# Kernel optimization log

Hardware: AMD Instinct MI355X
Metric: run time of the kernel (lower is better)

Reference implementation:

```python
import jax, jax.numpy as jnp
import numpy as np

N, E, D_IN, H, OUT = 50000, 800000, 128, 256, 2
BN_EPS = 1e-5
LN_EPS = 1e-5


def _xavier(k, fi, fo):
    lim = float(np.sqrt(6.0 / (fi + fo)))
    return jax.random.uniform(k, (fi, fo), minval=-lim, maxval=lim, dtype=jnp.float32)


def setup_inputs() -> dict:
    key = jax.random.key(0)
    ks = jax.random.split(key, 8)
    return {
        "x": jax.random.normal(ks[0], (N, D_IN), dtype=jnp.float32),
        "edge_index": jax.random.randint(ks[1], (2, E), 0, N, dtype=jnp.int32),
        "feature_scale": jnp.ones((D_IN,), jnp.float32),
        "feature_bias": jnp.zeros((D_IN,), jnp.float32),
        "bn0_g": jnp.ones((D_IN,), jnp.float32),
        "bn0_b": jnp.zeros((D_IN,), jnp.float32),
        "W1": _xavier(ks[2], D_IN, H), "b1": jnp.zeros((H,), jnp.float32),
        "bn1_g": jnp.ones((H,), jnp.float32), "bn1_b": jnp.zeros((H,), jnp.float32),
        "ln1_g": jnp.ones((H,), jnp.float32), "ln1_b": jnp.zeros((H,), jnp.float32),
        "W2": _xavier(ks[3], H, H), "b2": jnp.zeros((H,), jnp.float32),
        "bn2_g": jnp.ones((H,), jnp.float32), "bn2_b": jnp.zeros((H,), jnp.float32),
        "ln2_g": jnp.ones((H,), jnp.float32), "ln2_b": jnp.zeros((H,), jnp.float32),
        "Wout": _xavier(ks[4], H, OUT), "bout": jnp.zeros((OUT,), jnp.float32),
    }


def _batchnorm(x, g, b):
    # training-mode BatchNorm1d: batch stats over node axis, biased variance
    mu = jnp.mean(x, axis=0)
    var = jnp.mean(jnp.square(x - mu), axis=0)
    return g * (x - mu) * jax.lax.rsqrt(var + BN_EPS) + b


def _layernorm(x, g, b):
    mu = jnp.mean(x, axis=-1, keepdims=True)
    var = jnp.mean(jnp.square(x - mu), axis=-1, keepdims=True)
    return g * (x - mu) * jax.lax.rsqrt(var + LN_EPS) + b


def _gcn(x, W, b, src, dst, dinv):
    # PyG GCNConv with self-loops: D^{-1/2}(A+I)D^{-1/2} X W + b
    h = x @ W                                   # [N, F]
    norm = (dinv[src] * dinv[dst])[:, None]     # [E, 1]
    msg = h[src] * norm                         # [E, F] (dominant traffic)
    agg = jax.ops.segment_sum(msg, dst, num_segments=N)
    return agg + (dinv * dinv)[:, None] * h + b


def _forward(x, feature_scale, feature_bias, bn0_g, bn0_b,
             W1, b1, bn1_g, bn1_b, ln1_g, ln1_b,
             W2, b2, bn2_g, bn2_b, ln2_g, ln2_b,
             Wout, bout, edge_index):
    src, dst = edge_index[0], edge_index[1]
    deg = jax.ops.segment_sum(jnp.ones((E,), x.dtype), dst, num_segments=N) + 1.0
    dinv = jax.lax.rsqrt(deg)

    h = x * feature_scale + feature_bias
    h = _batchnorm(h, bn0_g, bn0_b)            # input_bn; dropout = identity (eval)

    # layer 0 (no residual: i == 0)
    h1 = _gcn(h, W1, b1, src, dst, dinv)
    h1 = jax.nn.relu(h1)
    h1 = _batchnorm(h1, bn1_g, bn1_b)
    h1 = _layernorm(h1, ln1_g, ln1_b)

    # layer 1 (residual add, shapes match)
    h2 = _gcn(h1, W2, b2, src, dst, dinv)
    h2 = jax.nn.relu(h2)
    h2 = _batchnorm(h2, bn2_g, bn2_b)
    h2 = _layernorm(h2, ln2_g, ln2_b)
    h2 = h2 + h1

    return h2 @ Wout + bout


def reference(x, edge_index, feature_scale, feature_bias, bn0_g, bn0_b,
              W1, b1, bn1_g, bn1_b, ln1_g, ln1_b,
              W2, b2, bn2_g, bn2_b, ln2_g, ln2_b,
              Wout, bout):
    return _forward(x, feature_scale, feature_bias, bn0_g, bn0_b,
                    W1, b1, bn1_g, bn1_b, ln1_g, ln1_b,
                    W2, b2, bn2_g, bn2_b, ln2_g, ln2_b,
                    Wout, bout, edge_index)
```

## Files before the change

kernel.cpp:

```cpp
#include <hip/hip_runtime.h>
#include <hip/hip_bf16.h>
#include <stdint.h>

#define N_NODES 50000
#define N_EDGES 800000
#define D_IN    128
#define H_DIM   256
#define BN_EPS  1e-5f
#define LN_EPS  1e-5f
#define NBLK2 782
#define SLICE_ELEMS ((size_t)N_NODES * 32)
#define EDGE_CHUNK 4096
#define BN0_BLOCKS 1024
#define PREPX_BLOCKS 6250
#define TR_BLOCKS 256
#define NBKT 196
#define CHUNK 2048
#define RCHUNKS 391

typedef float v4f __attribute__((ext_vector_type(4)));
typedef float v2f __attribute__((ext_vector_type(2)));
typedef short v8s __attribute__((ext_vector_type(8)));
typedef unsigned v4u __attribute__((ext_vector_type(4)));

__device__ __forceinline__ float bflo(unsigned u){ return __uint_as_float(u << 16); }
__device__ __forceinline__ float bfhi(unsigned u){ return __uint_as_float(u & 0xffff0000u); }
__device__ __forceinline__ unsigned short f2bf(float f){
  unsigned u = __float_as_uint(f);
  u += 0x7fffu + ((u >> 16) & 1u);
  return (unsigned short)(u >> 16);
}
__device__ __forceinline__ unsigned pack2(float a, float b){
  return (unsigned)f2bf(a) | ((unsigned)f2bf(b) << 16);
}

__device__ __forceinline__ int block_excl_scan(int v){
  int t = threadIdx.x;
  int lane = t & 63, w = t >> 6;
  int inc = v;
  #pragma unroll
  for (int m = 1; m < 64; m <<= 1){
    int o = __shfl_up(inc, m, 64);
    if (lane >= m) inc += o;
  }
  __shared__ int wsum[4];
  if (lane == 63) wsum[w] = inc;
  __syncthreads();
  int base = 0;
  #pragma unroll
  for (int j = 0; j < 4; ++j) if (j < w) base += wsum[j];
  return base + inc - v;
}

__global__ __launch_bounds__(256) void bn0r1_k(const int* ei, const float* x,
                                               const float* fs, const float* fb,
                                               float* S, float* Q, int* ghist){
  int b = blockIdx.x, t = threadIdx.x;
  if (b >= BN0_BLOCKS){
    __shared__ int lh[NBKT];
    int b2 = b - BN0_BLOCKS;
    for (int i = t; i < NBKT; i += 256) lh[i] = 0;
    __syncthreads();
    int e0 = b2 * CHUNK;
    int n = min(CHUNK, N_EDGES - e0);
    for (int i = t; i < n; i += 256)
      atomicAdd(&lh[ei[N_EDGES + e0 + i] >> 8], 1);
    __syncthreads();
    if (t < NBKT && lh[t] > 0) atomicAdd(&ghist[t], lh[t]);
    return;
  }
  int cl = t & 31, rg = t >> 5;
  int c = cl * 4;
  float4 fs4 = *(const float4*)(fs + c);
  float4 fb4 = *(const float4*)(fb + c);
  float s0=0,s1=0,s2=0,s3=0,q0=0,q1=0,q2=0,q3=0;
  for (int row = b * 8 + rg; row < N_NODES; row += BN0_BLOCKS * 8){
    float4 xv = *(const float4*)(x + (size_t)row * D_IN + c);
    float v0 = xv.x * fs4.x + fb4.x;
    float v1 = xv.y * fs4.y + fb4.y;
    float v2 = xv.z * fs4.z + fb4.z;
    float v3 = xv.w * fs4.w + fb4.w;
    s0 += v0; s1 += v1; s2 += v2; s3 += v3;
    q0 += v0*v0; q1 += v1*v1; q2 += v2*v2; q3 += v3*v3;
  }
  __shared__ float red[256][8];
  red[t][0]=s0; red[t][1]=s1; red[t][2]=s2; red[t][3]=s3;
  red[t][4]=q0; red[t][5]=q1; red[t][6]=q2; red[t][7]=q3;
  __syncthreads();
  float* Sr = S + (b & 7) * D_IN;
  float* Qr = Q + (b & 7) * D_IN;
  if (t < 32){
    float a[8];
    #pragma unroll
    for (int i = 0; i < 8; ++i) a[i] = red[t][i];
    for (int j = 1; j < 8; ++j)
      #pragma unroll
      for (int i = 0; i < 8; ++i) a[i] += red[t + 32*j][i];
    #pragma unroll
    for (int i = 0; i < 4; ++i){ atomicAdd(&Sr[t*4+i], a[i]); atomicAdd(&Qr[t*4+i], a[4+i]); }
  }
}

__global__ __launch_bounds__(256) void r3_k(const int* ei, const int* ghist, int* gcursor, unsigned* ebuf){
  __shared__ unsigned short dstS[CHUNK];
  __shared__ int lh[NBKT], cb[NBKT], sbb[NBKT];
  int t = threadIdx.x;
  int v = (t < NBKT) ? ghist[t] : 0;
  int epre = block_excl_scan(v);
  if (t < NBKT){ sbb[t] = epre; lh[t] = 0; }
  __syncthreads();
  int e0 = blockIdx.x * CHUNK;
  int n = min(CHUNK, N_EDGES - e0);
  for (int i = t; i < n; i += 256){
    int d = ei[N_EDGES + e0 + i];
    dstS[i] = (unsigned short)d;
    atomicAdd(&lh[d >> 8], 1);
  }
  __syncthreads();
  if (t < NBKT && lh[t] > 0) cb[t] = sbb[t] + atomicAdd(&gcursor[t], lh[t]);
  __syncthreads();
  if (t < NBKT) lh[t] = 0;
  __syncthreads();
  for (int i = t; i < n; i += 256){
    int d = dstS[i];
    int bkt = d >> 8;
    int r = atomicAdd(&lh[bkt], 1);
    unsigned src = (unsigned)ei[e0 + i];
    ebuf[cb[bkt] + r] = ((unsigned)(d & 255) << 16) | src;
  }
}

__global__ __launch_bounds__(256) void sortprep_k(const unsigned* ebuf, const int* ghist,
                                                  int* perm, int* offs, float* dinv,
                                                  unsigned short* edges,
                                                  const float* x, const float* S, const float* Q,
                                                  const float* fs, const float* fb,
                                                  const float* gg, const float* bb,
                                                  unsigned short* xt,
                                                  const float* W1, const float* W2,
                                                  unsigned short* W1t, unsigned short* W2t){
  int b = blockIdx.x, t = threadIdx.x;
  if (b < NBKT){
    __shared__ int h[256], dh[128], ep_s[128], W_s[128], lc[128], curs[256], sbb[NBKT + 1];
    int gv = (t < NBKT) ? ghist[t] : 0;
    int gpre = block_excl_scan(gv);
    if (t < NBKT) sbb[t] = gpre;
    if (t == NBKT - 1) sbb[NBKT] = gpre + gv;
    h[t] = 0;
    if (t < 128){ dh[t] = 0; lc[t] = 0; }
    __syncthreads();
    int lo = sbb[b], hi = sbb[b + 1];
    for (int i = lo + t; i < hi; i += 256)
      atomicAdd(&h[(ebuf[i] >> 16) & 255], 1);
    __syncthreads();
    int node = b * 256 + t;
    bool valid = node < N_NODES;
    int deg = valid ? h[t] : 0;
    if (valid) atomicAdd(&dh[min(deg, 127)], 1);
    __syncthreads();
    int cv = (t < 128) ? dh[t] : 0;
    int e1 = block_excl_scan(cv);
    __syncthreads();
    int e2 = block_excl_scan((t < 128) ? cv * t : 0);
    __syncthreads();
    if (t < 128){ ep_s[t] = e1; W_s[t] = e2; }
    __syncthreads();
    if (valid){
      int bin = min(deg, 127);
      int r = atomicAdd(&lc[bin], 1);
      int pl = ep_s[bin] + r;
      int pos = b * 256 + pl;
      int off = lo + W_s[bin] + (pl - ep_s[bin]) * deg;
      perm[pos] = node;
      offs[pos] = off;
      dinv[node] = rsqrtf((float)deg + 1.0f);
      curs[t] = off;
    }
    __syncthreads();
    for (int i = lo + t; i < hi; i += 256){
      unsigned u = ebuf[i];
      int l8 = (u >> 16) & 255;
      int pos = atomicAdd(&curs[l8], 1);
      edges[pos] = (unsigned short)(u & 0xffffu);
    }
    if (b == 0 && t == 0) offs[N_NODES] = N_EDGES;
    return;
  }
  if (b < NBKT + PREPX_BLOCKS){
    int i = (b - NBKT) * 256 + t;
    int row = i >> 5; int c = (i & 31) * 4;
    float4 Sv = *(const float4*)(S + c);
    float4 Qv = *(const float4*)(Q + c);
    #pragma unroll
    for (int rep = 1; rep < 8; ++rep){
      float4 s2 = *(const float4*)(S + rep * D_IN + c);
      float4 q2 = *(const float4*)(Q + rep * D_IN + c);
      Sv.x += s2.x; Sv.y += s2.y; Sv.z += s2.z; Sv.w += s2.w;
      Qv.x += q2.x; Qv.y += q2.y; Qv.z += q2.z; Qv.w += q2.w;
    }
    float4 fs4 = *(const float4*)(fs + c);
    float4 fb4 = *(const float4*)(fb + c);
    float4 gg4 = *(const float4*)(gg + c);
    float4 bb4 = *(const float4*)(bb + c);
    const float invN = 1.0f / N_NODES;
    float mu0 = Sv.x*invN, mu1 = Sv.y*invN, mu2 = Sv.z*invN, mu3 = Sv.w*invN;
    float r0 = rsqrtf(Qv.x*invN - mu0*mu0 + BN_EPS);
    float r1 = rsqrtf(Qv.y*invN - mu1*mu1 + BN_EPS);
    float r2 = rsqrtf(Qv.z*invN - mu2*mu2 + BN_EPS);
    float r3 = rsqrtf(Qv.w*invN - mu3*mu3 + BN_EPS);
    float a0 = gg4.x*r0*fs4.x, c0 = gg4.x*r0*(fb4.x - mu0) + bb4.x;
    float a1 = gg4.y*r1*fs4.y, c1 = gg4.y*r1*(fb4.y - mu1) + bb4.y;
    float a2 = gg4.z*r2*fs4.z, c2 = gg4.z*r2*(fb4.z - mu2) + bb4.z;
    float a3 = gg4.w*r3*fs4.w, c3 = gg4.w*r3*(fb4.w - mu3) + bb4.w;
    float4 xv = *(const float4*)(x + (size_t)row * D_IN + c);
    uint2 o;
    o.x = pack2(a0 * xv.x + c0, a1 * xv.y + c1);
    o.y = pack2(a2 * xv.z + c2, a3 * xv.w + c3);
    *(uint2*)(xt + (size_t)row * D_IN + c) = o;
    return;
  }
  int i = (b - NBKT - PREPX_BLOCKS) * 256 + t;
  if (i < D_IN * H_DIM){
    int r = i / H_DIM, c = i % H_DIM;
    W1t[c * D_IN + r] = f2bf(W1[i]);
  }
  if (i < H_DIM * H_DIM){
    int r = i / H_DIM, c = i % H_DIM;
    W2t[c * H_DIM + r] = f2bf(W2[i]);
  }
}

template<int K>
__global__ __launch_bounds__(256) void gemm_k(const unsigned short* A, const unsigned short* Bt,
                                              const float* dinv, unsigned short* C, int M){
  __shared__ __align__(16) short smem[16896];
  __shared__ float dvs[64];
  short* As = smem;
  short* Bs = smem + 64 * 40;
  int t = threadIdx.x;
  int m0 = blockIdx.x * 64;
  int lane = t & 63;
  int w = t >> 6;
  int fr = lane & 15, quad = lane >> 4;
  if (t < 64) dvs[t] = (m0 + t < M) ? dinv[m0 + t] : 0.0f;
  v4f acc[4][4] = {};
  int sr = t >> 2;
  int sk = (t & 3) << 3;
  for (int k0 = 0; k0 < K; k0 += 32){
    __syncthreads();
    uint4 av = {0,0,0,0};
    int arow = m0 + sr;
    if (arow < M) av = *(const uint4*)(A + (size_t)arow * K + k0 + sk);
    *(uint4*)(&As[sr * 40 + sk]) = av;
    #pragma unroll
    for (int j = 0; j < 4; ++j){
      int brow = sr + 64 * j;
      uint4 bv = *(const uint4*)(Bt + (size_t)brow * K + k0 + sk);
      *(uint4*)(&Bs[brow * 40 + sk]) = bv;
    }
    __syncthreads();
    v8s af[4], bf[4];
    #pragma unroll
    for (int mi = 0; mi < 4; ++mi)
      af[mi] = *(const v8s*)(&As[(mi * 16 + fr) * 40 + quad * 8]);
    #pragma unroll
    for (int ni = 0; ni < 4; ++ni)
      bf[ni] = *(const v8s*)(&Bs[(w * 64 + ni * 16 + fr) * 40 + quad * 8]);
    #pragma unroll
    for (int mi = 0; mi < 4; ++mi)
      #pragma unroll
      for (int ni = 0; ni < 4; ++ni)
        acc[mi][ni] = __builtin_amdgcn_mfma_f32_16x16x32_bf16(af[mi], bf[ni], acc[mi][ni], 0, 0, 0);
  }
  __syncthreads();
  short* Cs = smem;
  #pragma unroll
  for (int mi = 0; mi < 4; ++mi)
    #pragma unroll
    for (int ni = 0; ni < 4; ++ni)
      #pragma unroll
      for (int r = 0; r < 4; ++r){
        int row = mi * 16 + quad * 4 + r;
        int col = w * 64 + ni * 16 + fr;
        Cs[row * 264 + col] = (short)f2bf(acc[mi][ni][r] * dvs[row]);
      }
  __syncthreads();
  int orow = t >> 2;
  int grow = m0 + orow;
  if (grow < M){
    #pragma unroll
    for (int j = 0; j < 4; ++j){
      int oc = (t & 3) * 16 + 64 * j;
      v8s v0 = *(const v8s*)(&Cs[orow * 264 + oc]);
      v8s v1 = *(const v8s*)(&Cs[orow * 264 + oc + 8]);
      *(v8s*)(&C[(size_t)(oc >> 5) * SLICE_ELEMS + (size_t)grow * 32 + (oc & 31)]) = v0;
      int oc1 = oc + 8;
      *(v8s*)(&C[(size_t)(oc1 >> 5) * SLICE_ELEMS + (size_t)grow * 32 + (oc1 & 31)]) = v1;
    }
  }
}

#define ACCP(u, A) { v2f d_ = {bflo(u), bfhi(u)}; A += d_; }
#define ACC8(vv) ACCP(vv.x, A0) ACCP(vv.y, A1) ACCP(vv.z, A2) ACCP(vv.w, A3)

__global__ __launch_bounds__(256, 4) void agg_k(const unsigned short* hs, const int* offsets,
                                                const unsigned short* edges, const int* perm,
                                                const float* dinv, const float* bias,
                                                unsigned short* g, float* pS, float* pQ){
  __shared__ unsigned eds32[EDGE_CHUNK / 2];
  __shared__ float wps[4][4][16];
  int t = threadIdx.x;
  int lane = t & 63;
  int wv = t >> 6;
  int slice = blockIdx.x & 7;
  int l4 = lane & 3;
  int grp = blockIdx.x >> 3;
  int nb = grp * 64;
  int idx = nb + (t >> 2);
  int lastn = min(nb + 64, N_NODES);
  int blk0 = offsets[nb];
  int base = blk0 & ~1;
  int blkN = offsets[lastn];
  const unsigned* gsrc = (const unsigned*)(edges + base);
  int nu = min((blkN - base + 1) >> 1, EDGE_CHUNK / 2);
  for (int i = t; i < nu; i += 256)
    eds32[i] = gsrc[i];
  __syncthreads();
  bool act = idx < N_NODES;
  int node = act ? perm[idx] : 0;
  float dvv = act ? dinv[node] : 0.f;
  const uint4* hb4 = (const uint4*)(hs + (size_t)slice * SLICE_ELEMS);
  float4 bb0 = *(const float4*)(bias + slice * 32 + l4 * 8);
  float4 bb1 = *(const float4*)(bias + slice * 32 + l4 * 8 + 4);
  uint4 sv = hb4[(size_t)node * 4 + l4];
  v2f A0 = {bflo(sv.x), bfhi(sv.x)};
  v2f A1 = {bflo(sv.y), bfhi(sv.y)};
  v2f A2 = {bflo(sv.z), bfhi(sv.z)};
  v2f A3 = {bflo(sv.w), bfhi(sv.w)};
  int e  = act ? offsets[idx] : 0;
  int e1 = act ? offsets[idx + 1] : 0;
  if ((e & 1) && e < e1){
    int ru = (e - base) >> 1;
    unsigned d = (ru < EDGE_CHUNK / 2) ? eds32[ru] : gsrc[ru];
    uint4 vv = hb4[(size_t)(d >> 16) * 4 + l4];
    ACC8(vv);
    ++e;
  }
  for (; e + 16 <= e1; e += 16){
    int ru = (e - base) >> 1;
    unsigned dd[8];
    if (ru + 8 <= EDGE_CHUNK / 2){
      #pragma unroll
      for (int j = 0; j < 8; ++j) dd[j] = eds32[ru + j];
    } else {
      #pragma unroll
      for (int j = 0; j < 8; ++j) dd[j] = gsrc[ru + j];
    }
    uint4 v[16];
    #pragma unroll
    for (int j = 0; j < 8; ++j){
      v[2*j]   = hb4[(size_t)(dd[j] & 0xffffu) * 4 + l4];
      v[2*j+1] = hb4[(size_t)(dd[j] >> 16)     * 4 + l4];
    }
    #pragma unroll
    for (int j = 0; j < 16; ++j){ ACC8(v[j]); }
  }
  if (e + 8 <= e1){
    int ru = (e - base) >> 1;
    unsigned dd[4];
    if (ru + 4 <= EDGE_CHUNK / 2){
      #pragma unroll
      for (int j = 0; j < 4; ++j) dd[j] = eds32[ru + j];
    } else {
      #pragma unroll
      for (int j = 0; j < 4; ++j) dd[j] = gsrc[ru + j];
    }
    uint4 v[8];
    #pragma unroll
    for (int j = 0; j < 4; ++j){
      v[2*j]   = hb4[(size_t)(dd[j] & 0xffffu) * 4 + l4];
      v[2*j+1] = hb4[(size_t)(dd[j] >> 16)     * 4 + l4];
    }
    #pragma unroll
    for (int j = 0; j < 8; ++j){ ACC8(v[j]); }
    e += 8;
  }
  if (e + 4 <= e1){
    int ru = (e - base) >> 1;
    unsigned dd0, dd1;
    if (ru + 2 <= EDGE_CHUNK / 2){
      dd0 = eds32[ru]; dd1 = eds32[ru + 1];
    } else {
      dd0 = gsrc[ru]; dd1 = gsrc[ru + 1];
    }
    uint4 v[4];
    v[0] = hb4[(size_t)(dd0 & 0xffffu) * 4 + l4];
    v[1] = hb4[(size_t)(dd0 >> 16)     * 4 + l4];
    v[2] = hb4[(size_t)(dd1 & 0xffffu) * 4 + l4];
    v[3] = hb4[(size_t)(dd1 >> 16)     * 4 + l4];
    #pragma unroll
    for (int j = 0; j < 4; ++j){ ACC8(v[j]); }
    e += 4;
  }
  for (; e < e1; ++e){
    int r = e - base;
    unsigned d = ((r >> 1) < EDGE_CHUNK / 2) ? eds32[r >> 1] : gsrc[r >> 1];
    unsigned s = (r & 1) ? (d >> 16) : (d & 0xffffu);
    uint4 vv = hb4[(size_t)s * 4 + l4];
    ACC8(vv);
  }
  float y0 = act ? fmaxf(dvv * A0.x + bb0.x, 0.f) : 0.f;
  float y1 = act ? fmaxf(dvv * A0.y + bb0.y, 0.f) : 0.f;
  float y2 = act ? fmaxf(dvv * A1.x + bb0.z, 0.f) : 0.f;
  float y3 = act ? fmaxf(dvv * A1.y + bb0.w, 0.f) : 0.f;
  float y4 = act ? fmaxf(dvv * A2.x + bb1.x, 0.f) : 0.f;
  float y5 = act ? fmaxf(dvv * A2.y + bb1.y, 0.f) : 0.f;
  float y6 = act ? fmaxf(dvv * A3.x + bb1.z, 0.f) : 0.f;
  float y7 = act ? fmaxf(dvv * A3.y + bb1.w, 0.f) : 0.f;
  if (act){
    v4u o;
    o.x = pack2(y0, y1); o.y = pack2(y2, y3);
    o.z = pack2(y4, y5); o.w = pack2(y6, y7);
    __builtin_nontemporal_store(o, (v4u*)(g + (size_t)node * H_DIM + slice * 32 + l4 * 8));
  }
  float q0 = y0*y0, q1 = y1*y1, q2 = y2*y2, q3 = y3*y3;
  float q4 = y4*y4, q5 = y5*y5, q6 = y6*y6, q7 = y7*y7;
  #pragma unroll
  for (int m = 4; m < 64; m <<= 1){
    y0 += __shfl_xor(y0, m, 64); y1 += __shfl_xor(y1, m, 64);
    y2 += __shfl_xor(y2, m, 64); y3 += __shfl_xor(y3, m, 64);
    y4 += __shfl_xor(y4, m, 64); y5 += __shfl_xor(y5, m, 64);
    y6 += __shfl_xor(y6, m, 64); y7 += __shfl_xor(y7, m, 64);
    q0 += __shfl_xor(q0, m, 64); q1 += __shfl_xor(q1, m, 64);
    q2 += __shfl_xor(q2, m, 64); q3 += __shfl_xor(q3, m, 64);
    q4 += __shfl_xor(q4, m, 64); q5 += __shfl_xor(q5, m, 64);
    q6 += __shfl_xor(q6, m, 64); q7 += __shfl_xor(q7, m, 64);
  }
  if (lane < 4){
    wps[wv][lane][0] = y0; wps[wv][lane][1] = y1; wps[wv][lane][2] = y2; wps[wv][lane][3] = y3;
    wps[wv][lane][4] = y4; wps[wv][lane][5] = y5; wps[wv][lane][6] = y6; wps[wv][lane][7] = y7;
    wps[wv][lane][8] = q0; wps[wv][lane][9] = q1; wps[wv][lane][10] = q2; wps[wv][lane][11] = q3;
    wps[wv][lane][12] = q4; wps[wv][lane][13] = q5; wps[wv][lane][14] = q6; wps[wv][lane][15] = q7;
  }
  __syncthreads();
  if (t < 64){
    int tl = t >> 4, ti = t & 15;
    float v = wps[0][tl][ti] + wps[1][tl][ti] + wps[2][tl][ti] + wps[3][tl][ti];
    int col32 = tl * 8 + (ti & 7);
    if (ti < 8) pS[(size_t)blockIdx.x * 32 + col32] = v;
    else        pQ[(size_t)blockIdx.x * 32 + col32] = v;
  }
}

__global__ __launch_bounds__(1024) void redu_k(const float* pS, const float* pQ,
                                               float* Sg, float* Qg){
  __shared__ float ls[32][32], lq[32][32];
  int t = threadIdx.x;
  int slice = blockIdx.x & 7;
  int part = blockIdx.x >> 3;
  int grp = t >> 5, c32 = t & 31;
  float as = 0.f, aq = 0.f;
  for (int b2 = part + grp * 8; b2 < NBLK2; b2 += 256){
    size_t o = ((size_t)b2 * 8 + slice) * 32 + c32;
    as += pS[o]; aq += pQ[o];
  }
  ls[grp][c32] = as; lq[grp][c32] = aq;
  __syncthreads();
  if (t < 32){
    float S = 0.f, Q = 0.f;
    #pragma unroll
    for (int gI = 0; gI < 32; ++gI){ S += ls[gI][t]; Q += lq[gI][t]; }
    atomicAdd(&Sg[slice * 32 + t], S);
    atomicAdd(&Qg[slice * 32 + t], Q);
  }
}

__global__ __launch_bounds__(256) void apply1_k(const unsigned short* g,
                                                const float* Sg, const float* Qg,
                                                const float* bng, const float* bnb,
                                                const float* lng, const float* lnb, unsigned short* h1){
  int t = threadIdx.x;
  int lane32 = t & 31;
  int row = blockIdx.x * 8 + (t >> 5);
  if (row >= N_NODES) return;
  int c = lane32 * 8;
  const float invN = 1.0f / N_NODES;
  float4 S0 = *(const float4*)(Sg + c), S1 = *(const float4*)(Sg + c + 4);
  float4 Q0 = *(const float4*)(Qg + c), Q1 = *(const float4*)(Qg + c + 4);
  float4 G0 = *(const float4*)(bng + c), G1 = *(const float4*)(bng + c + 4);
  float4 B0 = *(const float4*)(bnb + c), B1 = *(const float4*)(bnb + c + 4);
  float Sa[8] = {S0.x,S0.y,S0.z,S0.w,S1.x,S1.y,S1.z,S1.w};
  float Qa[8] = {Q0.x,Q0.y,Q0.z,Q0.w,Q1.x,Q1.y,Q1.z,Q1.w};
  float Ga[8] = {G0.x,G0.y,G0.z,G0.w,G1.x,G1.y,G1.z,G1.w};
  float Ba[8] = {B0.x,B0.y,B0.z,B0.w,B1.x,B1.y,B1.z,B1.w};
  float scv[8], shv[8];
  #pragma unroll
  for (int j = 0; j < 8; ++j){
    float mu = Sa[j] * invN;
    float rs = rsqrtf(Qa[j] * invN - mu * mu + BN_EPS);
    float s = Ga[j] * rs;
    scv[j] = s; shv[j] = Ba[j] - s * mu;
  }
  uint4 u = *(const uint4*)(g + (size_t)row * H_DIM + c);
  float v0 = scv[0] * bflo(u.x) + shv[0];
  float v1 = scv[1] * bfhi(u.x) + shv[1];
  float v2 = scv[2] * bflo(u.y) + shv[2];
  float v3 = scv[3] * bfhi(u.y) + shv[3];
  float v4 = scv[4] * bflo(u.z) + shv[4];
  float v5 = scv[5] * bfhi(u.z) + shv[5];
  float v6 = scv[6] * bflo(u.w) + shv[6];
  float v7 = scv[7] * bfhi(u.w) + shv[7];
  float sum = v0+v1+v2+v3+v4+v5+v6+v7;
  float sq  = v0*v0+v1*v1+v2*v2+v3*v3+v4*v4+v5*v5+v6*v6+v7*v7;
  #pragma unroll
  for (int m = 1; m < 32; m <<= 1){ sum += __shfl_xor(sum, m, 64); sq += __shfl_xor(sq, m, 64); }
  float mu = sum * (1.0f / H_DIM);
  float var = sq * (1.0f / H_DIM) - mu * mu;
  float rs = rsqrtf(var + LN_EPS);
  float4 g40 = *(const float4*)(lng + c);
  float4 g41 = *(const float4*)(lng + c + 4);
  float4 b40 = *(const float4*)(lnb + c);
  float4 b41 = *(const float4*)(lnb + c + 4);
  uint4 o;
  o.x = pack2(g40.x * (v0 - mu) * rs + b40.x, g40.y * (v1 - mu) * rs + b40.y);
  o.y = pack2(g40.z * (v2 - mu) * rs + b40.z, g40.w * (v3 - mu) * rs + b40.w);
  o.z = pack2(g41.x * (v4 - mu) * rs + b41.x, g41.y * (v5 - mu) * rs + b41.y);
  o.w = pack2(g41.z * (v6 - mu) * rs + b41.z, g41.w * (v7 - mu) * rs + b41.w);
  *(uint4*)(h1 + (size_t)row * H_DIM + c) = o;
}

__global__ __launch_bounds__(256) void apply2_k(const unsigned short* g,
                                                const float* Sg, const float* Qg,
                                                const float* bng, const float* bnb,
                                                const float* lng, const float* lnb,
                                                const unsigned short* h1, const float* Wout,
                                                const float* bout, float* out){
  int t = threadIdx.x;
  int lane32 = t & 31;
  int row = blockIdx.x * 8 + (t >> 5);
  if (row >= N_NODES) return;
  int c = lane32 * 8;
  const float invN = 1.0f / N_NODES;
  float4 S0 = *(const float4*)(Sg + c), S1 = *(const float4*)(Sg + c + 4);
  float4 Q0 = *(const float4*)(Qg + c), Q1 = *(const float4*)(Qg + c + 4);
  float4 G0 = *(const float4*)(bng + c), G1 = *(const float4*)(bng + c + 4);
  float4 B0 = *(const float4*)(bnb + c), B1 = *(const float4*)(bnb + c + 4);
  float Sa[8] = {S0.x,S0.y,S0.z,S0.w,S1.x,S1.y,S1.z,S1.w};
  float Qa[8] = {Q0.x,Q0.y,Q0.z,Q0.w,Q1.x,Q1.y,Q1.z,Q1.w};
  float Ga[8] = {G0.x,G0.y,G0.z,G0.w,G1.x,G1.y,G1.z,G1.w};
  float Ba[8] = {B0.x,B0.y,B0.z,B0.w,B1.x,B1.y,B1.z,B1.w};
  float scv[8], shv[8];
  #pragma unroll
  for (int j = 0; j < 8; ++j){
    float mu = Sa[j] * invN;
    float rs = rsqrtf(Qa[j] * invN - mu * mu + BN_EPS);
    float s = Ga[j] * rs;
    scv[j] = s; shv[j] = Ba[j] - s * mu;
  }
  uint4 u = *(const uint4*)(g + (size_t)row * H_DIM + c);
  float v0 = scv[0] * bflo(u.x) + shv[0];
  float v1 = scv[1] * bfhi(u.x) + shv[1];
  float v2 = scv[2] * bflo(u.y) + shv[2];
  float v3 = scv[3] * bfhi(u.y) + shv[3];
  float v4 = scv[4] * bflo(u.z) + shv[4];
  float v5 = scv[5] * bfhi(u.z) + shv[5];
  float v6 = scv[6] * bflo(u.w) + shv[6];
  float v7 = scv[7] * bfhi(u.w) + shv[7];
  float sum = v0+v1+v2+v3+v4+v5+v6+v7;
  float sq  = v0*v0+v1*v1+v2*v2+v3*v3+v4*v4+v5*v5+v6*v6+v7*v7;
  #pragma unroll
  for (int m = 1; m < 32; m <<= 1){ sum += __shfl_xor(sum, m, 64); sq += __shfl_xor(sq, m, 64); }
  float mu = sum * (1.0f / H_DIM);
  float var = sq * (1.0f / H_DIM) - mu * mu;
  float rs = rsqrtf(var + LN_EPS);
  float4 g40 = *(const float4*)(lng + c);
  float4 g41 = *(const float4*)(lng + c + 4);
  float4 b40 = *(const float4*)(lnb + c);
  float4 b41 = *(const float4*)(lnb + c + 4);
  uint4 hr = *(const uint4*)(h1 + (size_t)row * H_DIM + c);
  float y0 = g40.x * (v0 - mu) * rs + b40.x + bflo(hr.x);
  float y1 = g40.y * (v1 - mu) * rs + b40.y + bfhi(hr.x);
  float y2 = g40.z * (v2 - mu) * rs + b40.z + bflo(hr.y);
  float y3 = g40.w * (v3 - mu) * rs + b40.w + bfhi(hr.y);
  float y4 = g41.x * (v4 - mu) * rs + b41.x + bflo(hr.z);
  float y5 = g41.y * (v5 - mu) * rs + b41.y + bfhi(hr.z);
  float y6 = g41.z * (v6 - mu) * rs + b41.z + bflo(hr.w);
  float y7 = g41.w * (v7 - mu) * rs + b41.w + bfhi(hr.w);
  float4 w0 = *(const float4*)(Wout + c * 2);
  float4 w1 = *(const float4*)(Wout + c * 2 + 4);
  float4 w2 = *(const float4*)(Wout + c * 2 + 8);
  float4 w3 = *(const float4*)(Wout + c * 2 + 12);
  float o0 = y0*w0.x + y1*w0.z + y2*w1.x + y3*w1.z + y4*w2.x + y5*w2.z + y6*w3.x + y7*w3.z;
  float o1 = y0*w0.y + y1*w0.w + y2*w1.y + y3*w1.w + y4*w2.y + y5*w2.w + y6*w3.y + y7*w3.w;
  #pragma unroll
  for (int m = 1; m < 32; m <<= 1){ o0 += __shfl_xor(o0, m, 64); o1 += __shfl_xor(o1, m, 64); }
  if (lane32 == 0){
    out[(size_t)row * 2 + 0] = o0 + bout[0];
    out[(size_t)row * 2 + 1] = o1 + bout[1];
  }
}

extern "C" void kernel_launch(void* const* d_in, const int* in_sizes, int n_in,
                              void* d_out, int out_size, void* d_ws, size_t ws_size,
                              hipStream_t stream) {
  const float* x    = (const float*)d_in[0];
  const int*   ei   = (const int*)d_in[1];
  const float* fs   = (const float*)d_in[2];
  const float* fb   = (const float*)d_in[3];
  const float* bn0g = (const float*)d_in[4];
  const float* bn0b = (const float*)d_in[5];
  const float* W1   = (const float*)d_in[6];
  const float* b1   = (const float*)d_in[7];
  const float* bn1g = (const float*)d_in[8];
  const float* bn1b = (const float*)d_in[9];
  const float* ln1g = (const float*)d_in[10];
  const float* ln1b = (const float*)d_in[11];
  const float* W2   = (const float*)d_in[12];
  const float* b2   = (const float*)d_in[13];
  const float* bn2g = (const float*)d_in[14];
  const float* bn2b = (const float*)d_in[15];
  const float* ln2g = (const float*)d_in[16];
  const float* ln2b = (const float*)d_in[17];
  const float* Wout = (const float*)d_in[18];
  const float* bout = (const float*)d_in[19];
  float* out = (float*)d_out;

  char* w = (char*)d_ws;
  float* bn0S  = (float*)(w + 0);
  float* bn0Q  = (float*)(w + 4096);
  int*   ghist  = (int*)(w + 8192);
  int*   gcursor= (int*)(w + 8976);
  float* Sg1   = (float*)(w + 9760);
  float* Qg1   = (float*)(w + 10784);
  float* Sg2   = (float*)(w + 11808);
  float* Qg2   = (float*)(w + 12832);
  const size_t ZERO_BYTES = 13856;
  float* dinv  = (float*)(w + 211584);
  int*   offs  = (int*)(w + 411584);
  int*   perm  = (int*)(w + 611712);
  unsigned short* edges = (unsigned short*)(w + 1011712);
  unsigned short* xt   = (unsigned short*)(w + 2611712);
  unsigned short* W1t  = (unsigned short*)(w + 15411712);
  unsigned short* W2t  = (unsigned short*)(w + 15477248);
  unsigned short* hlin = (unsigned short*)(w + 15608320);
  unsigned*       ebuf = (unsigned*)(w + 15608320);
  unsigned short* gbuf = (unsigned short*)(w + 41208320);
  unsigned short* h1   = (unsigned short*)(w + 66808320);
  float* pS    = (float*)(w + 92408320);
  float* pQ    = (float*)(w + 94008832);

  (void)in_sizes; (void)n_in; (void)out_size; (void)ws_size;

  hipMemsetAsync(d_ws, 0, ZERO_BYTES, stream);

  bn0r1_k<<<BN0_BLOCKS + RCHUNKS, 256, 0, stream>>>(ei, x, fs, fb, bn0S, bn0Q, ghist);
  r3_k<<<RCHUNKS, 256, 0, stream>>>(ei, ghist, gcursor, ebuf);
  sortprep_k<<<NBKT + PREPX_BLOCKS + TR_BLOCKS, 256, 0, stream>>>(
      ebuf, ghist, perm, offs, dinv, edges, x, bn0S, bn0Q, fs, fb, bn0g, bn0b, xt, W1, W2, W1t, W2t);

  int ggrid = (N_NODES + 63) / 64;
  int agg_blocks = NBLK2 * 8;

  gemm_k<D_IN><<<ggrid, 256, 0, stream>>>(xt, W1t, dinv, hlin, N_NODES);
  agg_k<<<agg_blocks, 256, 0, stream>>>(hlin, offs, edges, perm, dinv, b1, gbuf, pS, pQ);
  redu_k<<<64, 1024, 0, stream>>>(pS, pQ, Sg1, Qg1);
  apply1_k<<<(N_NODES + 7) / 8, 256, 0, stream>>>(gbuf, Sg1, Qg1, bn1g, bn1b, ln1g, ln1b, h1);

  gemm_k<H_DIM><<<ggrid, 256, 0, stream>>>(h1, W2t, dinv, hlin, N_NODES);
  agg_k<<<agg_blocks, 256, 0, stream>>>(hlin, offs, edges, perm, dinv, b2, gbuf, pS, pQ);
  redu_k<<<64, 1024, 0, stream>>>(pS, pQ, Sg2, Qg2);
  apply2_k<<<(N_NODES + 7) / 8, 256, 0, stream>>>(gbuf, Sg2, Qg2, bn2g, bn2b, ln2g, ln2b, h1, Wout, bout, out);
}
```

Before: 337.8 us.

## Fuse input BN prep into GEMM1 and BN/LN apply into GEMM2 prologue

The separate pass that normalised x into a bf16 buffer is removed, and GEMM1 now loads fp32 x, applies the folded scale and bias, and stages the whole 64x128 A tile in shared memory. The apply1 kernel is removed too. GEMM2 now reads the aggregated rows, applies BatchNorm and LayerNorm in its prologue, keeps the full 64x256 A tile in LDS, and also writes h1 for the later residual. This removes two kernel launches and the write and re-read of intermediate buffers, at the cost of larger LDS use per block (lower occupancy) and heavy per-thread register use in the GEMM2 prologue.

```diff
diff --git a/kernel.cpp b/kernel.cpp
--- a/kernel.cpp
+++ b/kernel.cpp
@@ -12,7 +12,6 @@
 #define SLICE_ELEMS ((size_t)N_NODES * 32)
 #define EDGE_CHUNK 4096
 #define BN0_BLOCKS 1024
-#define PREPX_BLOCKS 6250
 #define TR_BLOCKS 256
 #define NBKT 196
 #define CHUNK 2048
@@ -133,10 +132,6 @@
 __global__ __launch_bounds__(256) void sortprep_k(const unsigned* ebuf, const int* ghist,
                                                   int* perm, int* offs, float* dinv,
                                                   unsigned short* edges,
-                                                  const float* x, const float* S, const float* Q,
-                                                  const float* fs, const float* fb,
-                                                  const float* gg, const float* bb,
-                                                  unsigned short* xt,
                                                   const float* W1, const float* W2,
                                                   unsigned short* W1t, unsigned short* W2t){
   int b = blockIdx.x, t = threadIdx.x;
@@ -186,40 +181,7 @@
     if (b == 0 && t == 0) offs[N_NODES] = N_EDGES;
     return;
   }
-  if (b < NBKT + PREPX_BLOCKS){
-    int i = (b - NBKT) * 256 + t;
-    int row = i >> 5; int c = (i & 31) * 4;
-    float4 Sv = *(const float4*)(S + c);
-    float4 Qv = *(const float4*)(Q + c);
-    #pragma unroll
-    for (int rep = 1; rep < 8; ++rep){
-      float4 s2 = *(const float4*)(S + rep * D_IN + c);
-      float4 q2 = *(const float4*)(Q + rep * D_IN + c);
-      Sv.x += s2.x; Sv.y += s2.y; Sv.z += s2.z; Sv.w += s2.w;
-      Qv.x += q2.x; Qv.y += q2.y; Qv.z += q2.z; Qv.w += q2.w;
-    }
-    float4 fs4 = *(const float4*)(fs + c);
-    float4 fb4 = *(const float4*)(fb + c);
-    float4 gg4 = *(const float4*)(gg + c);
-    float4 bb4 = *(const float4*)(bb + c);
-    const float invN = 1.0f / N_NODES;
-    float mu0 = Sv.x*invN, mu1 = Sv.y*invN, mu2 = Sv.z*invN, mu3 = Sv.w*invN;
-    float r0 = rsqrtf(Qv.x*invN - mu0*mu0 + BN_EPS);
-    float r1 = rsqrtf(Qv.y*invN - mu1*mu1 + BN_EPS);
-    float r2 = rsqrtf(Qv.z*invN - mu2*mu2 + BN_EPS);
-    float r3 = rsqrtf(Qv.w*invN - mu3*mu3 + BN_EPS);
-    float a0 = gg4.x*r0*fs4.x, c0 = gg4.x*r0*(fb4.x - mu0) + bb4.x;
-    float a1 = gg4.y*r1*fs4.y, c1 = gg4.y*r1*(fb4.y - mu1) + bb4.y;
-    float a2 = gg4.z*r2*fs4.z, c2 = gg4.z*r2*(fb4.z - mu2) + bb4.z;
-    float a3 = gg4.w*r3*fs4.w, c3 = gg4.w*r3*(fb4.w - mu3) + bb4.w;
-    float4 xv = *(const float4*)(x + (size_t)row * D_IN + c);
-    uint2 o;
-    o.x = pack2(a0 * xv.x + c0, a1 * xv.y + c1);
-    o.y = pack2(a2 * xv.z + c2, a3 * xv.w + c3);
-    *(uint2*)(xt + (size_t)row * D_IN + c) = o;
-    return;
-  }
-  int i = (b - NBKT - PREPX_BLOCKS) * 256 + t;
+  int i = (b - NBKT) * 256 + t;
   if (i < D_IN * H_DIM){
     int r = i / H_DIM, c = i % H_DIM;
     W1t[c * D_IN + r] = f2bf(W1[i]);
@@ -230,39 +192,194 @@
   }
 }
 
-template<int K>
-__global__ __launch_bounds__(256) void gemm_k(const unsigned short* A, const unsigned short* Bt,
-                                              const float* dinv, unsigned short* C, int M){
-  __shared__ __align__(16) short smem[16896];
-  __shared__ float dvs[64];
+__global__ __launch_bounds__(256) void gemm1_k(const float* x, const float* S, const float* Q,
+                                               const float* fs, const float* fb,
+                                               const float* gg, const float* bb,
+                                               const unsigned short* Bt, const float* dinv,
+                                               unsigned short* C, int M){
+  __shared__ __align__(16) short smem[18944];
+  __shared__ float ac[128], cc[128], dvs[64];
   short* As = smem;
-  short* Bs = smem + 64 * 40;
+  short* Bs = smem + 64 * 136;
   int t = threadIdx.x;
   int m0 = blockIdx.x * 64;
-  int lane = t & 63;
-  int w = t >> 6;
+  int lane = t & 63, w = t >> 6;
   int fr = lane & 15, quad = lane >> 4;
   if (t < 64) dvs[t] = (m0 + t < M) ? dinv[m0 + t] : 0.0f;
+  if (t < 128){
+    float s8 = 0.f, q8 = 0.f;
+    #pragma unroll
+    for (int rep = 0; rep < 8; ++rep){ s8 += S[rep * D_IN + t]; q8 += Q[rep * D_IN + t]; }
+    const float invN = 1.0f / N_NODES;
+    float mu = s8 * invN;
+    float rs = rsqrtf(q8 * invN - mu * mu + BN_EPS);
+    float a = gg[t] * rs * fs[t];
+    ac[t] = a;
+    cc[t] = gg[t] * rs * (fb[t] - mu) + bb[t];
+  }
+  __syncthreads();
+  {
+    int r = t >> 2, q = t & 3;
+    int arow = m0 + r;
+    #pragma unroll
+    for (int j = 0; j < 4; ++j){
+      int c = q * 32 + j * 8;
+      float4 xv0 = {0,0,0,0}, xv1 = {0,0,0,0};
+      if (arow < M){
+        xv0 = *(const float4*)(x + (size_t)arow * D_IN + c);
+        xv1 = *(const float4*)(x + (size_t)arow * D_IN + c + 4);
+      }
+      float4 a0 = *(const float4*)(&ac[c]);
+      float4 a1 = *(const float4*)(&ac[c + 4]);
+      float4 c0 = *(const float4*)(&cc[c]);
+      float4 c1 = *(const float4*)(&cc[c + 4]);
+      uint4 o;
+      o.x = pack2(a0.x * xv0.x + c0.x, a0.y * xv0.y + c0.y);
+      o.y = pack2(a0.z * xv0.z + c0.z, a0.w * xv0.w + c0.w);
+      o.z = pack2(a1.x * xv1.x + c1.x, a1.y * xv1.y + c1.y);
+      o.w = pack2(a1.z * xv1.z + c1.z, a1.w * xv1.w + c1.w);
+      *(uint4*)(&As[r * 136 + c]) = o;
+    }
+  }
   v4f acc[4][4] = {};
   int sr = t >> 2;
   int sk = (t & 3) << 3;
-  for (int k0 = 0; k0 < K; k0 += 32){
-    __syncthreads();
-    uint4 av = {0,0,0,0};
-    int arow = m0 + sr;
-    if (arow < M) av = *(const uint4*)(A + (size_t)arow * K + k0 + sk);
-    *(uint4*)(&As[sr * 40 + sk]) = av;
+  for (int k0 = 0; k0 < D_IN; k0 += 32){
+    __syncthreads();
     #pragma unroll
     for (int j = 0; j < 4; ++j){
       int brow = sr + 64 * j;
-      uint4 bv = *(const uint4*)(Bt + (size_t)brow * K + k0 + sk);
+      uint4 bv = *(const uint4*)(Bt + (size_t)brow * D_IN + k0 + sk);
       *(uint4*)(&Bs[brow * 40 + sk]) = bv;
     }
     __syncthreads();
     v8s af[4], bf[4];
     #pragma unroll
     for (int mi = 0; mi < 4; ++mi)
-      af[mi] = *(const v8s*)(&As[(mi * 16 + fr) * 40 + quad * 8]);
+      af[mi] = *(const v8s*)(&As[(mi * 16 + fr) * 136 + k0 + quad * 8]);
+    #pragma unroll
+    for (int ni = 0; ni < 4; ++ni)
+      bf[ni] = *(const v8s*)(&Bs[(w * 64 + ni * 16 + fr) * 40 + quad * 8]);
+    #pragma unroll
+    for (int mi = 0; mi < 4; ++mi)
+      #pragma unroll
+      for (int ni = 0; ni < 4; ++ni)
+        acc[mi][ni] = __builtin_amdgcn_mfma_f32_16x16x32_bf16(af[mi], bf[ni], acc[mi][ni], 0, 0, 0);
+  }
+  __syncthreads();
+  short* Cs = smem;
+  #pragma unroll
+  for (int mi = 0; mi < 4; ++mi)
+    #pragma unroll
+    for (int ni = 0; ni < 4; ++ni)
+      #pragma unroll
+      for (int r = 0; r < 4; ++r){
+        int row = mi * 16 + quad * 4 + r;
+        int col = w * 64 + ni * 16 + fr;
+        Cs[row * 264 + col] = (short)f2bf(acc[mi][ni][r] * dvs[row]);
+      }
+  __syncthreads();
+  int orow = t >> 2;
+  int grow = m0 + orow;
+  if (grow < M){
+    #pragma unroll
+    for (int j = 0; j < 4; ++j){
+      int oc = (t & 3) * 16 + 64 * j;
+      v8s v0 = *(const v8s*)(&Cs[orow * 264 + oc]);
+      v8s v1 = *(const v8s*)(&Cs[orow * 264 + oc + 8]);
+      *(v8s*)(&C[(size_t)(oc >> 5) * SLICE_ELEMS + (size_t)grow * 32 + (oc & 31)]) = v0;
+      int oc1 = oc + 8;
+      *(v8s*)(&C[(size_t)(oc1 >> 5) * SLICE_ELEMS + (size_t)grow * 32 + (oc1 & 31)]) = v1;
+    }
+  }
+}
+
+__global__ __launch_bounds__(256) void gemm2_k(const unsigned short* gB,
+                                               const float* Sg, const float* Qg,
+                                               const float* bng, const float* bnb,
+                                               const float* lng, const float* lnb,
+                                               const unsigned short* Bt, const float* dinv,
+                                               unsigned short* C, unsigned short* h1, int M){
+  __shared__ __align__(16) short smem[27136];
+  __shared__ float scs[256], shs[256], dvs[64];
+  short* As = smem;
+  short* Bs = smem + 64 * 264;
+  int t = threadIdx.x;
+  int m0 = blockIdx.x * 64;
+  int lane = t & 63, w = t >> 6;
+  int fr = lane & 15, quad = lane >> 4;
+  if (t < 64) dvs[t] = (m0 + t < M) ? dinv[m0 + t] : 0.0f;
+  {
+    const float invN = 1.0f / N_NODES;
+    float mu = Sg[t] * invN;
+    float rs = rsqrtf(Qg[t] * invN - mu * mu + BN_EPS);
+    float s = bng[t] * rs;
+    scs[t] = s; shs[t] = bnb[t] - s * mu;
+  }
+  __syncthreads();
+  {
+    int r = t >> 2, q = t & 3;
+    int grow = m0 + r;
+    int c0 = q * 64;
+    float v[64];
+    #pragma unroll
+    for (int j = 0; j < 8; ++j){
+      uint4 u = {0,0,0,0};
+      int c = c0 + j * 8;
+      if (grow < M) u = *(const uint4*)(gB + (size_t)grow * H_DIM + c);
+      float4 s0 = *(const float4*)(&scs[c]);
+      float4 s1 = *(const float4*)(&scs[c + 4]);
+      float4 h0 = *(const float4*)(&shs[c]);
+      float4 h4 = *(const float4*)(&shs[c + 4]);
+      v[j*8+0] = s0.x * bflo(u.x) + h0.x;
+      v[j*8+1] = s0.y * bfhi(u.x) + h0.y;
+      v[j*8+2] = s0.z * bflo(u.y) + h0.z;
+      v[j*8+3] = s0.w * bfhi(u.y) + h0.w;
+      v[j*8+4] = s1.x * bflo(u.z) + h4.x;
+      v[j*8+5] = s1.y * bfhi(u.z) + h4.y;
+      v[j*8+6] = s1.z * bflo(u.w) + h4.z;
+      v[j*8+7] = s1.w * bfhi(u.w) + h4.w;
+    }
+    float sum = 0.f, sq = 0.f;
+    #pragma unroll
+    for (int i = 0; i < 64; ++i){ sum += v[i]; sq += v[i] * v[i]; }
+    sum += __shfl_xor(sum, 1, 64); sum += __shfl_xor(sum, 2, 64);
+    sq  += __shfl_xor(sq, 1, 64);  sq  += __shfl_xor(sq, 2, 64);
+    float mu = sum * (1.0f / H_DIM);
+    float var = sq * (1.0f / H_DIM) - mu * mu;
+    float rs = rsqrtf(var + LN_EPS);
+    #pragma unroll
+    for (int j = 0; j < 8; ++j){
+      int c = c0 + j * 8;
+      float4 g0 = *(const float4*)(lng + c);
+      float4 g1 = *(const float4*)(lng + c + 4);
+      float4 b0 = *(const float4*)(lnb + c);
+      float4 b1 = *(const float4*)(lnb + c + 4);
+      uint4 o;
+      o.x = pack2(g0.x * (v[j*8+0] - mu) * rs + b0.x, g0.y * (v[j*8+1] - mu) * rs + b0.y);
+      o.y = pack2(g0.z * (v[j*8+2] - mu) * rs + b0.z, g0.w * (v[j*8+3] - mu) * rs + b0.w);
+      o.z = pack2(g1.x * (v[j*8+4] - mu) * rs + b1.x, g1.y * (v[j*8+5] - mu) * rs + b1.y);
+      o.w = pack2(g1.z * (v[j*8+6] - mu) * rs + b1.z, g1.w * (v[j*8+7] - mu) * rs + b1.w);
+      *(uint4*)(&As[r * 264 + c]) = o;
+      if (grow < M) *(uint4*)(h1 + (size_t)grow * H_DIM + c) = o;
+    }
+  }
+  v4f acc[4][4] = {};
+  int sr = t >> 2;
+  int sk = (t & 3) << 3;
+  for (int k0 = 0; k0 < H_DIM; k0 += 32){
+    __syncthreads();
+    #pragma unroll
+    for (int j = 0; j < 4; ++j){
+      int brow = sr + 64 * j;
+      uint4 bv = *(const uint4*)(Bt + (size_t)brow * H_DIM + k0 + sk);
+      *(uint4*)(&Bs[brow * 40 + sk]) = bv;
+    }
+    __syncthreads();
+    v8s af[4], bf[4];
+    #pragma unroll
+    for (int mi = 0; mi < 4; ++mi)
+      af[mi] = *(const v8s*)(&As[(mi * 16 + fr) * 264 + k0 + quad * 8]);
     #pragma unroll
     for (int ni = 0; ni < 4; ++ni)
       bf[ni] = *(const v8s*)(&Bs[(w * 64 + ni * 16 + fr) * 40 + quad * 8]);
@@ -473,60 +590,6 @@
     atomicAdd(&Sg[slice * 32 + t], S);
     atomicAdd(&Qg[slice * 32 + t], Q);
   }
-}
-
-__global__ __launch_bounds__(256) void apply1_k(const unsigned short* g,
-                                                const float* Sg, const float* Qg,
-                                                const float* bng, const float* bnb,
-                                                const float* lng, const float* lnb, unsigned short* h1){
-  int t = threadIdx.x;
-  int lane32 = t & 31;
-  int row = blockIdx.x * 8 + (t >> 5);
-  if (row >= N_NODES) return;
-  int c = lane32 * 8;
-  const float invN = 1.0f / N_NODES;
-  float4 S0 = *(const float4*)(Sg + c), S1 = *(const float4*)(Sg + c + 4);
-  float4 Q0 = *(const float4*)(Qg + c), Q1 = *(const float4*)(Qg + c + 4);
-  float4 G0 = *(const float4*)(bng + c), G1 = *(const float4*)(bng + c + 4);
-  float4 B0 = *(const float4*)(bnb + c), B1 = *(const float4*)(bnb + c + 4);
-  float Sa[8] = {S0.x,S0.y,S0.z,S0.w,S1.x,S1.y,S1.z,S1.w};
-  float Qa[8] = {Q0.x,Q0.y,Q0.z,Q0.w,Q1.x,Q1.y,Q1.z,Q1.w};
-  float Ga[8] = {G0.x,G0.y,G0.z,G0.w,G1.x,G1.y,G1.z,G1.w};
-  float Ba[8] = {B0.x,B0.y,B0.z,B0.w,B1.x,B1.y,B1.z,B1.w};
-  float scv[8], shv[8];
-  #pragma unroll
-  for (int j = 0; j < 8; ++j){
-    float mu = Sa[j] * invN;
-    float rs = rsqrtf(Qa[j] * invN - mu * mu + BN_EPS);
-    float s = Ga[j] * rs;
-    scv[j] = s; shv[j] = Ba[j] - s * mu;
-  }
-  uint4 u = *(const uint4*)(g + (size_t)row * H_DIM + c);
-  float v0 = scv[0] * bflo(u.x) + shv[0];
-  float v1 = scv[1] * bfhi(u.x) + shv[1];
-  float v2 = scv[2] * bflo(u.y) + shv[2];
-  float v3 = scv[3] * bfhi(u.y) + shv[3];
-  float v4 = scv[4] * bflo(u.z) + shv[4];
-  float v5 = scv[5] * bfhi(u.z) + shv[5];
-  float v6 = scv[6] * bflo(u.w) + shv[6];
-  float v7 = scv[7] * bfhi(u.w) + shv[7];
-  float sum = v0+v1+v2+v3+v4+v5+v6+v7;
-  float sq  = v0*v0+v1*v1+v2*v2+v3*v3+v4*v4+v5*v5+v6*v6+v7*v7;
-  #pragma unroll
-  for (int m = 1; m < 32; m <<= 1){ sum += __shfl_xor(sum, m, 64); sq += __shfl_xor(sq, m, 64); }
-  float mu = sum * (1.0f / H_DIM);
-  float var = sq * (1.0f / H_DIM) - mu * mu;
-  float rs = rsqrtf(var + LN_EPS);
-  float4 g40 = *(const float4*)(lng + c);
-  float4 g41 = *(const float4*)(lng + c + 4);
-  float4 b40 = *(const float4*)(lnb + c);
-  float4 b41 = *(const float4*)(lnb + c + 4);
-  uint4 o;
-  o.x = pack2(g40.x * (v0 - mu) * rs + b40.x, g40.y * (v1 - mu) * rs + b40.y);
-  o.y = pack2(g40.z * (v2 - mu) * rs + b40.z, g40.w * (v3 - mu) * rs + b40.w);
-  o.z = pack2(g41.x * (v4 - mu) * rs + b41.x, g41.y * (v5 - mu) * rs + b41.y);
-  o.w = pack2(g41.z * (v6 - mu) * rs + b41.z, g41.w * (v7 - mu) * rs + b41.w);
-  *(uint4*)(h1 + (size_t)row * H_DIM + c) = o;
 }
 
 __global__ __launch_bounds__(256) void apply2_k(const unsigned short* g,
@@ -639,7 +702,6 @@
   int*   offs  = (int*)(w + 411584);
   int*   perm  = (int*)(w + 611712);
   unsigned short* edges = (unsigned short*)(w + 1011712);
-  unsigned short* xt   = (unsigned short*)(w + 2611712);
   unsigned short* W1t  = (unsigned short*)(w + 15411712);
   unsigned short* W2t  = (unsigned short*)(w + 15477248);
   unsigned short* hlin = (unsigned short*)(w + 15608320);
@@ -655,18 +717,17 @@
 
   bn0r1_k<<<BN0_BLOCKS + RCHUNKS, 256, 0, stream>>>(ei, x, fs, fb, bn0S, bn0Q, ghist);
   r3_k<<<RCHUNKS, 256, 0, stream>>>(ei, ghist, gcursor, ebuf);
-  sortprep_k<<<NBKT + PREPX_BLOCKS + TR_BLOCKS, 256, 0, stream>>>(
-      ebuf, ghist, perm, offs, dinv, edges, x, bn0S, bn0Q, fs, fb, bn0g, bn0b, xt, W1, W2, W1t, W2t);
+  sortprep_k<<<NBKT + TR_BLOCKS, 256, 0, stream>>>(
+      ebuf, ghist, perm, offs, dinv, edges, W1, W2, W1t, W2t);
 
   int ggrid = (N_NODES + 63) / 64;
   int agg_blocks = NBLK2 * 8;
 
-  gemm_k<D_IN><<<ggrid, 256, 0, stream>>>(xt, W1t, dinv, hlin, N_NODES);
+  gemm1_k<<<ggrid, 256, 0, stream>>>(x, bn0S, bn0Q, fs, fb, bn0g, bn0b, W1t, dinv, hlin, N_NODES);
   agg_k<<<agg_blocks, 256, 0, stream>>>(hlin, offs, edges, perm, dinv, b1, gbuf, pS, pQ);
   redu_k<<<64, 1024, 0, stream>>>(pS, pQ, Sg1, Qg1);
-  apply1_k<<<(N_NODES + 7) / 8, 256, 0, stream>>>(gbuf, Sg1, Qg1, bn1g, bn1b, ln1g, ln1b, h1);
-
-  gemm_k<H_DIM><<<ggrid, 256, 0, stream>>>(h1, W2t, dinv, hlin, N_NODES);
+
+  gemm2_k<<<ggrid, 256, 0, stream>>>(gbuf, Sg1, Qg1, bn1g, bn1b, ln1g, ln1b, W2t, dinv, hlin, h1, N_NODES);
   agg_k<<<agg_blocks, 256, 0, stream>>>(hlin, offs, edges, perm, dinv, b2, gbuf, pS, pQ);
   redu_k<<<64, 1024, 0, stream>>>(pS, pQ, Sg2, Qg2);
   apply2_k<<<(N_NODES + 7) / 8, 256, 0, stream>>>(gbuf, Sg2, Qg2, bn2g, bn2b, ln2g, ln2b, h1, Wout, bout, out);
```

New measurement: 360.3 us. 1.07x slower.
